# Kernel optimization log

Measured on AMD Instinct MI355X. Metric: run time of the kernel, lower is better.

The kernel has to match this reference:

```python
import jax, jax.numpy as jnp
import numpy as np

L_XYZ = 10  # fourier freqs for position -> 3 + 6*10 = 63 dims
L_DIR = 4   # fourier freqs for direction -> 3 + 6*4 = 27 dims
DIM = 32    # radiance feature dim per depth layer
PPP = 4     # points (depth layers) per pixel
HID = 128   # MLP hidden width
UCH = 64    # UNet hidden channels


def pe(x, L):
    # fourier positional encoding: [x, sin(2^k x), cos(2^k x)]
    f = (2.0 ** jnp.arange(L)).astype(x.dtype)
    xf = x[..., None] * f  # [..., 3, L]
    s = jnp.sin(xf).reshape(x.shape[:-1] + (-1,))
    c = jnp.cos(xf).reshape(x.shape[:-1] + (-1,))
    return jnp.concatenate([x, s, c], axis=-1)


def conv(x, w, b):
    y = jax.lax.conv_general_dilated(x, w, (1, 1), 'SAME',
                                     dimension_numbers=('NCHW', 'OIHW', 'NCHW'))
    return y + b[None, :, None, None]


def setup_inputs() -> dict:
    key = jax.random.key(0)
    ks = jax.random.split(key, 24)
    H = W = 384
    zbufs = jax.random.uniform(ks[0], (H, W, PPP), dtype=jnp.float32)  # depths in [0,1)
    o = jax.random.normal(ks[1], (H, W, 3), dtype=jnp.float32)
    d = jax.random.normal(ks[2], (H, W, 3), dtype=jnp.float32)
    d = d / jnp.linalg.norm(d, axis=-1, keepdims=True)
    cos = jax.random.uniform(ks[3], (H, W, 1), dtype=jnp.float32) * 0.5 + 0.5
    ray = jnp.concatenate([o, d, cos], axis=-1)  # [H,W,7]
    gt = jax.random.uniform(ks[4], (H, W, 3), dtype=jnp.float32)
    mask_gt = jnp.ones((H, W, 1), dtype=jnp.float32)
    xyz_o = jax.random.normal(ks[5], (1024, 3), dtype=jnp.float32)
    in_xyz = 3 + 6 * L_XYZ
    in_dir = 3 + 6 * L_DIR
    in_ch = DIM * PPP
    p = {}
    p['w1'] = jax.random.normal(ks[6], (in_xyz, HID), dtype=jnp.float32) * 0.05
    p['b1'] = jnp.zeros((HID,), dtype=jnp.float32)
    p['w2'] = jax.random.normal(ks[7], (HID, HID), dtype=jnp.float32) * 0.05
    p['b2'] = jnp.zeros((HID,), dtype=jnp.float32)
    p['w3'] = jax.random.normal(ks[8], (HID + in_dir, DIM), dtype=jnp.float32) * 0.05
    p['b3'] = jnp.zeros((DIM,), dtype=jnp.float32)
    p['mpn_w1'] = jax.random.normal(ks[9], (in_ch, in_ch, 3, 3), dtype=jnp.float32) * 0.02
    p['mpn_b1'] = jnp.zeros((in_ch,), dtype=jnp.float32)
    p['mpn_w2'] = jax.random.normal(ks[10], (in_ch, in_ch, 3, 3), dtype=jnp.float32) * 0.02
    p['mpn_b2'] = jnp.zeros((in_ch,), dtype=jnp.float32)
    p['uw1'] = jax.random.normal(ks[11], (UCH, in_ch, 3, 3), dtype=jnp.float32) * 0.02
    p['ub1'] = jnp.zeros((UCH,), dtype=jnp.float32)
    p['uw2'] = jax.random.normal(ks[12], (UCH, UCH, 3, 3), dtype=jnp.float32) * 0.02
    p['ub2'] = jnp.zeros((UCH,), dtype=jnp.float32)
    p['uw3'] = jax.random.normal(ks[13], (3, UCH, 3, 3), dtype=jnp.float32) * 0.02
    p['ub3'] = jnp.zeros((3,), dtype=jnp.float32)
    inp = {'zbufs': zbufs, 'ray': ray, 'gt': gt, 'mask_gt': mask_gt,
           'isTrain': 1, 'xyz_o': xyz_o}
    inp.update(p)
    return inp


def reference(zbufs, ray, gt, mask_gt, isTrain, xyz_o,
              w1, b1, w2, b2, w3, b3,
              mpn_w1, mpn_b1, mpn_w2, mpn_b2,
              uw1, ub1, uw2, ub2, uw3, ub3):
    H, W, P = zbufs.shape
    o = ray[..., :3]
    dirs = ray[..., 3:6]
    cos = ray[..., 6:7]
    thresh = 0.2 if isTrain else 0.0
    # dense equivalent of boolean-mask gather -> MLP -> scatter into zeros
    mask = (zbufs > thresh).astype(zbufs.dtype)  # [H,W,P]
    # xyz_near = o + dirs * zbuf / cos  (xyznear path)
    xyz = o[..., None, :] + dirs[..., None, :] * zbufs[..., None] / cos[..., None]  # [H,W,P,3]
    x = pe(xyz, L_XYZ)                                   # [H,W,P,63]
    h = jax.nn.relu(x @ w1 + b1)                         # [H,W,P,HID]
    h = jax.nn.relu(h @ w2 + b2)
    dpe = pe(dirs, L_DIR)                                # [H,W,27]
    dpe = jnp.broadcast_to(dpe[..., None, :], h.shape[:-1] + (dpe.shape[-1],))
    feat = jnp.concatenate([h, dpe], axis=-1) @ w3 + b3  # [H,W,P,DIM]
    feat = feat * mask[..., None]                        # zeros where pix_mask is False
    # per-layer permute(2,3,0,1) + cat(dim=1) == [1, P*DIM, H, W]
    rdmp = feat.transpose(2, 3, 0, 1).reshape(1, P * DIM, H, W)
    # MPN: predicted per-channel mask
    m = jax.nn.sigmoid(conv(jax.nn.relu(conv(rdmp, mpn_w1, mpn_b1)), mpn_w2, mpn_b2))
    fuse = rdmp * m
    fea_map = jax.nn.sigmoid(fuse[0, :3].transpose(1, 2, 0))  # [H,W,3]
    # UNet refinement to RGB
    u = jax.nn.relu(conv(fuse, uw1, ub1))
    u = jax.nn.relu(conv(u, uw2, ub2))
    img = jax.nn.sigmoid(conv(u, uw3, ub3))[0].transpose(1, 2, 0)  # [H,W,3]
    return img
```

## Files before the change

### kernel.cpp

```cpp
#include <hip/hip_runtime.h>
#include <hip/hip_bf16.h>
#include <math.h>

typedef __attribute__((ext_vector_type(8))) unsigned short ushort8;
typedef __attribute__((ext_vector_type(8))) __bf16 bf16x8;
typedef __attribute__((ext_vector_type(4))) float floatx4;

constexpr int IMGW = 384;
constexpr int NPIX = IMGW * IMGW;

__device__ __forceinline__ unsigned short f2bf(float f) {
  union { float f; unsigned u; } v; v.f = f;
  unsigned u = v.u;
  return (unsigned short)((u + 0x7fffu + ((u >> 16) & 1u)) >> 16);
}
__device__ __forceinline__ float bf2f(unsigned short h) {
  union { unsigned u; float f; } v; v.u = ((unsigned)h) << 16; return v.f;
}
__device__ __forceinline__ unsigned pk2bf(float a, float b) {
  float2 f2; f2.x = a; f2.y = b;
  __hip_bfloat162 h = __float22bfloat162_rn(f2);
  union { __hip_bfloat162 h; unsigned u; } u; u.h = h; return u.u;
}
__device__ __forceinline__ floatx4 mfma16(bf16x8 a, bf16x8 b, floatx4 c) {
  return __builtin_amdgcn_mfma_f32_16x16x32_bf16(a, b, c, 0, 0, 0);
}
__device__ __forceinline__ bf16x8 lds_frag(const unsigned short* p) {
  return *reinterpret_cast<const bf16x8*>(p);
}
__device__ __forceinline__ bf16x8 u4_to_bf(uint4 v) {
  union { uint4 u; bf16x8 b; } c; c.u = v; return c.b;
}

__device__ __forceinline__ void convB_elem(const float* __restrict__ w,
                                           unsigned short* __restrict__ wt,
                                           int i, int CIN, int G, int NT) {
  int j = i & 7, lane = (i >> 3) & 63;
  int rest = i >> 9;
  int nt = rest % NT; int rest2 = rest / NT;
  int g = rest2 % G;  int ks = rest2 / G;
  int q = lane >> 4, m = lane & 15;
  int co = (g * NT + nt) * 16 + m;
  int k = ks * 32 + q * 8 + j;
  int nb = k / CIN, ci = k - nb * CIN;
  wt[i] = f2bf(w[(co * CIN + ci) * 9 + nb]);
}

__global__ __launch_bounds__(256) void prep_all(
    const float* __restrict__ w1, const float* __restrict__ w2, const float* __restrict__ w3,
    const float* __restrict__ mw1, const float* __restrict__ mw2,
    const float* __restrict__ uw1, const float* __restrict__ uw2,
    unsigned short* __restrict__ w1A, unsigned short* __restrict__ w2A,
    unsigned short* __restrict__ w3A,
    unsigned short* __restrict__ cw1, unsigned short* __restrict__ cw2,
    unsigned short* __restrict__ cu1, unsigned short* __restrict__ cu2) {
  int i = blockIdx.x * 256 + threadIdx.x;
  if (i < 28672) {
    if (i < 8192) {
      int j = i & 7, lane = (i >> 3) & 63, t = i >> 9;
      int mt = t >> 1, ks = t & 1;
      int ch_out = mt * 16 + (lane & 15);
      int kp = ks * 32 + (lane >> 4) * 8 + j;
      int chunk = kp >> 3, sl = kp & 7;
      float val;
      if (chunk == 7 && sl >= 4) {
        int c = sl - 4;
        val = (c < 3) ? w1[c * 128 + ch_out] : 0.0f;
      } else {
        const int coordA[8] = {0,0,0,1,1,2,2,2};
        const int octA[8]   = {0,4,8,2,6,0,4,8};
        const int coordB[8] = {0,0,1,1,1,2,2,2};
        const int octB[8]   = {2,6,0,4,8,2,6,0};
        int rc  = (sl < 4) ? coordA[chunk] : coordB[chunk];
        int oct = ((sl < 4) ? octA[chunk] : octB[chunk]) + ((sl >> 1) & 1);
        int korig = ((sl & 1) ? 33 : 3) + rc * 10 + oct;
        val = w1[korig * 128 + ch_out];
      }
      w1A[i] = f2bf(val);
    } else if (i < 24576) {
      int i2 = i - 8192;
      int j = i2 & 7, lane = (i2 >> 3) & 63, t = i2 >> 9;
      int mt = t >> 2, ks = t & 3;
      int ch_out = mt * 16 + (lane & 15);
      int kp = ks * 32 + (lane >> 4) * 8 + j;
      int c_orig = ((kp >> 2) & 7) * 16 + (kp >> 5) * 4 + (kp & 3);
      w2A[i2] = f2bf(w2[c_orig * 128 + ch_out]);
    } else {
      int i3 = i - 24576;
      int j = i3 & 7, lane = (i3 >> 3) & 63, t = i3 >> 9;
      int mt = t >> 2, ks = t & 3;
      int ch_out = mt * 16 + (lane & 15);
      int kp = ks * 32 + (lane >> 4) * 8 + j;
      int c_orig = ((kp >> 2) & 7) * 16 + (kp >> 5) * 4 + (kp & 3);
      w3A[i3] = f2bf(w3[c_orig * 32 + ch_out]);
    }
    return;
  }
  i -= 28672;
  if (i < 147456) { convB_elem(mw1, cw1, i, 128, 4, 2); return; }
  i -= 147456;
  if (i < 147456) { convB_elem(mw2, cw2, i, 128, 4, 2); return; }
  i -= 147456;
  if (i < 73728)  { convB_elem(uw1, cu1, i, 128, 4, 1); return; }
  i -= 73728;
  if (i < 36864)  { convB_elem(uw2, cu2, i, 64, 4, 1); return; }
}

__global__ __launch_bounds__(256) void dcon_kernel(
    const float* __restrict__ ray, const float* __restrict__ w3,
    const float* __restrict__ b3, float* __restrict__ dconG) {
  int gid = blockIdx.x * 256 + threadIdx.x;
  int pixel = gid >> 5, c = gid & 31;
  const float* r = ray + (size_t)pixel * 7;
  float d0 = r[3], d1 = r[4], d2 = r[5];
  float acc = b3[c];
  acc += d0 * w3[128 * 32 + c] + d1 * w3[129 * 32 + c] + d2 * w3[130 * 32 + c];
  float dv[3] = { d0, d1, d2 };
  #pragma unroll
  for (int cc = 0; cc < 3; ++cc) {
    float fs = 1.0f;
    #pragma unroll
    for (int f = 0; f < 4; ++f) {
      float s, co;
      __sincosf(dv[cc] * fs, &s, &co);
      acc += s * w3[(131 + cc * 4 + f) * 32 + c];
      acc += co * w3[(143 + cc * 4 + f) * 32 + c];
      fs *= 2.0f;
    }
  }
  dconG[gid] = acc;
}

__global__ __launch_bounds__(64, 3) void mlp_kernel(
    const float* __restrict__ zbufs, const float* __restrict__ ray,
    const int* __restrict__ isTrain,
    const float* __restrict__ b1, const float* __restrict__ b2,
    const unsigned short* __restrict__ w1A, const unsigned short* __restrict__ w2A,
    const unsigned short* __restrict__ w3A, const float* __restrict__ dconG,
    unsigned short* __restrict__ rdmp) {
  __shared__ __align__(16) unsigned short H[64 * 136];

  const int lane = threadIdx.x;
  const int q = lane >> 4, m = lane & 15;
  const float thresh = (isTrain[0] != 0) ? 0.2f : 0.0f;

  float fA[2], fB[2];
  int cAi[2], cBi[2];
  #pragma unroll
  for (int half = 0; half < 2; ++half) {
    int ch = half * 4 + q;
    cAi[half] = (ch <= 2) ? 0 : ((ch <= 4) ? 1 : 2);
    fA[half]  = (ch == 0 || ch == 5) ? 1.0f :
                (ch == 1 || ch == 6) ? 16.0f :
                (ch == 2 || ch == 7) ? 256.0f :
                (ch == 3) ? 4.0f : 64.0f;
    cBi[half] = (ch <= 1) ? 0 : ((ch <= 4) ? 1 : 2);
    fB[half]  = (ch == 2) ? 1.0f :
                (ch == 0 || ch == 5) ? 4.0f :
                (ch == 3) ? 16.0f :
                (ch == 1 || ch == 6) ? 64.0f : 256.0f;
  }

  bf16x8 bx[4][2];
  float zs[4];
  #pragma unroll
  for (int nt = 0; nt < 4; ++nt) {
    int s = nt * 16 + m;
    int sg = blockIdx.x * 64 + s;
    int pixel = sg >> 2;
    float z = zbufs[sg];
    zs[nt] = z;
    const float* r = ray + (size_t)pixel * 7;
    float t = z / r[6];
    float xv0 = r[0] + r[3] * t, xv1 = r[1] + r[4] * t, xv2 = r[2] + r[5] * t;
    #pragma unroll
    for (int half = 0; half < 2; ++half) {
      float uA = (cAi[half] == 0) ? xv0 : ((cAi[half] == 1) ? xv1 : xv2);
      float uB = (cBi[half] == 0) ? xv0 : ((cBi[half] == 1) ? xv1 : xv2);
      float sa, ca, sb, cb;
      __sincosf(uA * fA[half], &sa, &ca);
      __sincosf(uB * fB[half], &sb, &cb);
      float t2a = sa + sa;
      float sa1 = t2a * ca, ca1 = fmaf(-t2a, sa, 1.0f);
      float t2b = sb + sb;
      float sb1 = t2b * cb, cb1 = fmaf(-t2b, sb, 1.0f);
      if (half == 1 && q == 3) { sb = xv0; cb = xv1; sb1 = xv2; cb1 = 0.0f; }
      uint4 dv;
      dv.x = pk2bf(sa, ca); dv.y = pk2bf(sa1, ca1);
      dv.z = pk2bf(sb, cb); dv.w = pk2bf(sb1, cb1);
      bx[nt][half] = u4_to_bf(dv);
    }
  }

  #pragma unroll 1
  for (int half = 0; half < 2; ++half) {
    floatx4 acc[4][4];
    #pragma unroll
    for (int mt = 0; mt < 4; ++mt) {
      float4 bb = *reinterpret_cast<const float4*>(b1 + (half * 4 + mt) * 16 + q * 4);
      #pragma unroll
      for (int nt = 0; nt < 4; ++nt) {
        acc[mt][nt][0] = bb.x; acc[mt][nt][1] = bb.y;
        acc[mt][nt][2] = bb.z; acc[mt][nt][3] = bb.w;
      }
    }
    #pragma unroll
    for (int ks = 0; ks < 2; ++ks) {
      #pragma unroll
      for (int mt = 0; mt < 4; ++mt) {
        int mtg = half * 4 + mt;
        bf16x8 a = *reinterpret_cast<const bf16x8*>(w1A + (((mtg << 1) + ks) << 9) + lane * 8);
        #pragma unroll
        for (int nt = 0; nt < 4; ++nt)
          acc[mt][nt] = mfma16(a, bx[nt][ks], acc[mt][nt]);
      }
    }
    #pragma unroll
    for (int nt = 0; nt < 4; ++nt) {
      uint4* base = reinterpret_cast<uint4*>(&H[(nt * 16 + m) * 136 + q * 32 + half * 16]);
      #pragma unroll
      for (int g = 0; g < 2; ++g) {
        uint4 v;
        v.x = pk2bf(fmaxf(acc[2*g][nt][0], 0.0f),   fmaxf(acc[2*g][nt][1], 0.0f));
        v.y = pk2bf(fmaxf(acc[2*g][nt][2], 0.0f),   fmaxf(acc[2*g][nt][3], 0.0f));
        v.z = pk2bf(fmaxf(acc[2*g+1][nt][0], 0.0f), fmaxf(acc[2*g+1][nt][1], 0.0f));
        v.w = pk2bf(fmaxf(acc[2*g+1][nt][2], 0.0f), fmaxf(acc[2*g+1][nt][3], 0.0f));
        base[g] = v;
      }
    }
  }

  {
    uint4 keep[4][2];
    #pragma unroll 1
    for (int half = 0; half < 2; ++half) {
      floatx4 acc[4][4];
      #pragma unroll
      for (int mt = 0; mt < 4; ++mt) {
        float4 bb = *reinterpret_cast<const float4*>(b2 + (half * 4 + mt) * 16 + q * 4);
        #pragma unroll
        for (int nt = 0; nt < 4; ++nt) {
          acc[mt][nt][0] = bb.x; acc[mt][nt][1] = bb.y;
          acc[mt][nt][2] = bb.z; acc[mt][nt][3] = bb.w;
        }
      }
      #pragma unroll 1
      for (int ks = 0; ks < 4; ++ks) {
        bf16x8 bf[4];
        #pragma unroll
        for (int nt = 0; nt < 4; ++nt)
          bf[nt] = lds_frag(H + (nt * 16 + m) * 136 + ks * 32 + q * 8);
        #pragma unroll
        for (int mt = 0; mt < 4; ++mt) {
          int mtg = half * 4 + mt;
          bf16x8 a = *reinterpret_cast<const bf16x8*>(w2A + (((mtg << 2) + ks) << 9) + lane * 8);
          #pragma unroll
          for (int nt = 0; nt < 4; ++nt)
            acc[mt][nt] = mfma16(a, bf[nt], acc[mt][nt]);
        }
      }
      #pragma unroll
      for (int nt = 0; nt < 4; ++nt) {
        #pragma unroll
        for (int g = 0; g < 2; ++g) {
          uint4 v;
          v.x = pk2bf(fmaxf(acc[2*g][nt][0], 0.0f),   fmaxf(acc[2*g][nt][1], 0.0f));
          v.y = pk2bf(fmaxf(acc[2*g][nt][2], 0.0f),   fmaxf(acc[2*g][nt][3], 0.0f));
          v.z = pk2bf(fmaxf(acc[2*g+1][nt][0], 0.0f), fmaxf(acc[2*g+1][nt][1], 0.0f));
          v.w = pk2bf(fmaxf(acc[2*g+1][nt][2], 0.0f), fmaxf(acc[2*g+1][nt][3], 0.0f));
          if (half == 0) {
            keep[nt][g] = v;
          } else {
            *reinterpret_cast<uint4*>(&H[(nt * 16 + m) * 136 + q * 32 + 16 + g * 8]) = v;
          }
        }
      }
    }
    #pragma unroll
    for (int nt = 0; nt < 4; ++nt)
      #pragma unroll
      for (int g = 0; g < 2; ++g)
        *reinterpret_cast<uint4*>(&H[(nt * 16 + m) * 136 + q * 32 + g * 8]) = keep[nt][g];
  }

  {
    floatx4 acc[2][4];
    const float* dg = dconG + (size_t)blockIdx.x * 512;
    #pragma unroll
    for (int nt = 0; nt < 4; ++nt) {
      int s = nt * 16 + m;
      #pragma unroll
      for (int mt = 0; mt < 2; ++mt)
        acc[mt][nt] = *reinterpret_cast<const floatx4*>(dg + (s >> 2) * 32 + mt * 16 + q * 4);
    }
    #pragma unroll 2
    for (int ks = 0; ks < 4; ++ks) {
      bf16x8 bf[4];
      #pragma unroll
      for (int nt = 0; nt < 4; ++nt)
        bf[nt] = lds_frag(H + (nt * 16 + m) * 136 + ks * 32 + q * 8);
      #pragma unroll
      for (int mt = 0; mt < 2; ++mt) {
        bf16x8 a = *reinterpret_cast<const bf16x8*>(w3A + (((mt << 2) + ks) << 9) + lane * 8);
        #pragma unroll
        for (int nt = 0; nt < 4; ++nt)
          acc[mt][nt] = mfma16(a, bf[nt], acc[mt][nt]);
      }
    }
    #pragma unroll
    for (int nt = 0; nt < 4; ++nt) {
      int s = nt * 16 + m;
      float mk = (zs[nt] > thresh) ? 1.0f : 0.0f;
      unsigned short* dst = rdmp + (size_t)blockIdx.x * 2048 + s * 32 + q * 4;
      #pragma unroll
      for (int mt = 0; mt < 2; ++mt) {
        uint2 pk;
        pk.x = pk2bf(acc[mt][nt][0] * mk, acc[mt][nt][1] * mk);
        pk.y = pk2bf(acc[mt][nt][2] * mk, acc[mt][nt][3] * mk);
        *reinterpret_cast<uint2*>(dst + mt * 16) = pk;
      }
    }
  }
}

template<int CIN, int COUT, int MODE, int MINW>
__global__ __launch_bounds__(256, MINW) void conv3x3(
    const unsigned short* __restrict__ in, const unsigned short* __restrict__ wt,
    const float* __restrict__ bias, const unsigned short* __restrict__ rdmp,
    unsigned short* __restrict__ out) {
  constexpr int CP  = CIN + 8;
  constexpr int CH8 = CIN / 8;
  constexpr int KC  = CIN / 32;
  constexpr int NT  = COUT / 64;
  constexpr int GROUPS = KC * 3;
  __shared__ __align__(16) unsigned short lds_in[10 * 18 * CP];

  const int tid = threadIdx.x;
  const int x0 = blockIdx.x * 16, y0 = blockIdx.y * 8;

  for (int i = tid; i < 180 * CH8; i += 256) {
    int pix = i / CH8, part = i - pix * CH8;
    int xx = pix % 18, yy = pix / 18;
    int gx = x0 - 1 + xx, gy = y0 - 1 + yy;
    ushort8 v = {0, 0, 0, 0, 0, 0, 0, 0};
    if (gx >= 0 && gx < IMGW && gy >= 0 && gy < IMGW)
      v = *reinterpret_cast<const ushort8*>(in + ((size_t)(gy * IMGW + gx)) * CIN + part * 8);
    *reinterpret_cast<ushort8*>(&lds_in[pix * CP + part * 8]) = v;
  }
  __syncthreads();

  const int wave = tid >> 6, lane = tid & 63, q = lane >> 4, m = lane & 15;
  floatx4 acc[8][NT] = {};

  auto loadB = [&](int g, bf16x8 (&bb)[3][NT]) {
    int kc = g / 3, dx = g - kc * 3;
    #pragma unroll
    for (int dy = 0; dy < 3; ++dy) {
      int ks = (dy * 3 + dx) * KC + kc;
      #pragma unroll
      for (int nt = 0; nt < NT; ++nt)
        bb[dy][nt] = *reinterpret_cast<const bf16x8*>(
            wt + ((((size_t)ks * 4 + wave) * NT + nt) << 9) + lane * 8);
    }
  };

  bf16x8 bcur[3][NT], bnxt[3][NT];
  loadB(0, bcur);

  #pragma unroll 1
  for (int g = 0; g < GROUPS; ++g) {
    if (g + 1 < GROUPS) loadB(g + 1, bnxt);
    int kc = g / 3, dx = g - kc * 3;
    bf16x8 a[10];
    #pragma unroll
    for (int rr = 0; rr < 10; ++rr)
      a[rr] = lds_frag(&lds_in[(rr * 18 + m + dx) * CP + kc * 32 + q * 8]);
    #pragma unroll
    for (int dy = 0; dy < 3; ++dy)
      #pragma unroll
      for (int nt = 0; nt < NT; ++nt)
        #pragma unroll
        for (int mt = 0; mt < 8; ++mt)
          acc[mt][nt] = mfma16(a[mt + dy], bcur[dy][nt], acc[mt][nt]);
    #pragma unroll
    for (int dy = 0; dy < 3; ++dy)
      #pragma unroll
      for (int nt = 0; nt < NT; ++nt)
        bcur[dy][nt] = bnxt[dy][nt];
  }

  const int co0 = wave * (COUT / 4);
  #pragma unroll
  for (int mt = 0; mt < 8; ++mt) {
    int y = y0 + mt;
    #pragma unroll
    for (int nt = 0; nt < NT; ++nt) {
      int co = co0 + nt * 16 + m;
      float bb = bias[co];
      #pragma unroll
      for (int r = 0; r < 4; ++r) {
        int pixel = y * IMGW + x0 + q * 4 + r;
        float v = acc[mt][nt][r] + bb;
        if (MODE == 0) {
          v = fmaxf(v, 0.0f);
        } else {
          v = 1.0f / (1.0f + __expf(-v));
          v *= bf2f(rdmp[(size_t)pixel * 128 + co]);
        }
        out[(size_t)pixel * COUT + co] = f2bf(v);
      }
    }
  }
}

__global__ __launch_bounds__(256) void uconv3_kernel(
    const unsigned short* __restrict__ u2, const float* __restrict__ w,
    const float* __restrict__ b, float* __restrict__ out) {
  __shared__ float wl[1728];
  for (int i = threadIdx.x; i < 1728; i += 256) {
    int c = i % 3; int t = i / 3; int ci = t & 63; int nb = t >> 6;
    wl[i] = w[(c * 64 + ci) * 9 + nb];
  }
  __syncthreads();
  int pixel = blockIdx.x * 256 + threadIdx.x;
  int py = pixel / IMGW, px = pixel - py * IMGW;
  float a0 = b[0], a1 = b[1], a2 = b[2];
  for (int nb = 0; nb < 9; ++nb) {
    int gy = py + nb / 3 - 1, gx = px + nb % 3 - 1;
    if (gx < 0 || gx >= IMGW || gy < 0 || gy >= IMGW) continue;
    const unsigned short* src = u2 + (size_t)(gy * IMGW + gx) * 64;
    const float* wp = wl + nb * 192;
    #pragma unroll
    for (int cc = 0; cc < 8; ++cc) {
      ushort8 v = *reinterpret_cast<const ushort8*>(src + cc * 8);
      #pragma unroll
      for (int j = 0; j < 8; ++j) {
        float uv = bf2f(v[j]);
        const float* w3p = wp + (cc * 8 + j) * 3;
        a0 += uv * w3p[0]; a1 += uv * w3p[1]; a2 += uv * w3p[2];
      }
    }
  }
  float* o = out + (size_t)pixel * 3;
  o[0] = 1.0f / (1.0f + __expf(-a0));
  o[1] = 1.0f / (1.0f + __expf(-a1));
  o[2] = 1.0f / (1.0f + __expf(-a2));
}

extern "C" void kernel_launch(void* const* d_in, const int* in_sizes, int n_in,
                              void* d_out, int out_size, void* d_ws, size_t ws_size,
                              hipStream_t stream) {
  (void)in_sizes; (void)n_in; (void)out_size; (void)ws_size;
  const float* zbufs = (const float*)d_in[0];
  const float* ray   = (const float*)d_in[1];
  const int* isTrain = (const int*)d_in[4];
  const float* w1 = (const float*)d_in[6];
  const float* b1 = (const float*)d_in[7];
  const float* w2 = (const float*)d_in[8];
  const float* b2 = (const float*)d_in[9];
  const float* w3 = (const float*)d_in[10];
  const float* b3 = (const float*)d_in[11];
  const float* mpn_w1 = (const float*)d_in[12];
  const float* mpn_b1 = (const float*)d_in[13];
  const float* mpn_w2 = (const float*)d_in[14];
  const float* mpn_b2 = (const float*)d_in[15];
  const float* uw1 = (const float*)d_in[16];
  const float* ub1 = (const float*)d_in[17];
  const float* uw2 = (const float*)d_in[18];
  const float* ub2 = (const float*)d_in[19];
  const float* uw3 = (const float*)d_in[20];
  const float* ub3 = (const float*)d_in[21];
  float* out = (float*)d_out;

  unsigned char* ws = (unsigned char*)d_ws;
  size_t off = 0;
  auto alloc = [&](size_t bytes) -> void* {
    void* p = ws + off; off = (off + bytes + 255) & ~(size_t)255; return p;
  };
  unsigned short* w1A  = (unsigned short*)alloc(8192 * 2);
  unsigned short* w2A  = (unsigned short*)alloc(16384 * 2);
  unsigned short* w3A  = (unsigned short*)alloc(4096 * 2);
  unsigned short* cw1  = (unsigned short*)alloc((size_t)128 * 1152 * 2);
  unsigned short* cw2  = (unsigned short*)alloc((size_t)128 * 1152 * 2);
  unsigned short* cu1  = (unsigned short*)alloc((size_t)64 * 1152 * 2);
  unsigned short* cu2  = (unsigned short*)alloc((size_t)64 * 576 * 2);
  unsigned short* rdmp = (unsigned short*)alloc((size_t)NPIX * 128 * 2);
  unsigned short* t1   = (unsigned short*)alloc((size_t)NPIX * 128 * 2);
  unsigned short* fuse = (unsigned short*)alloc((size_t)NPIX * 128 * 2);
  unsigned short* u1 = t1;
  unsigned short* u2 = rdmp;
  float* dconG = (float*)fuse;

  prep_all<<<1696, 256, 0, stream>>>(w1, w2, w3, mpn_w1, mpn_w2, uw1, uw2,
                                     w1A, w2A, w3A, cw1, cw2, cu1, cu2);
  dcon_kernel<<<NPIX * 32 / 256, 256, 0, stream>>>(ray, w3, b3, dconG);
  mlp_kernel<<<NPIX * 4 / 64, 64, 0, stream>>>(zbufs, ray, isTrain, b1, b2,
                                               w1A, w2A, w3A, dconG, rdmp);

  dim3 cgrid(IMGW / 16, IMGW / 8);
  conv3x3<128, 128, 0, 2><<<cgrid, 256, 0, stream>>>(rdmp, cw1, mpn_b1, nullptr, t1);
  conv3x3<128, 128, 1, 2><<<cgrid, 256, 0, stream>>>(t1, cw2, mpn_b2, rdmp, fuse);
  conv3x3<128, 64, 0, 3><<<cgrid, 256, 0, stream>>>(fuse, cu1, ub1, nullptr, u1);
  conv3x3<64, 64, 0, 3><<<cgrid, 256, 0, stream>>>(u1, cu2, ub2, nullptr, u2);
  uconv3_kernel<<<NPIX / 256, 256, 0, stream>>>(u2, uw3, ub3, out);
}
```

Before: 335.5 us.

## Split conv3x3 tile rows across 8 waves and double-buffer weight fragments

The 3x3 conv kernels now launch 512 threads per block. Waves are split into 4 output-channel groups by 2 row halves, so each wave accumulates 4 rows instead of 8. This halves per-wave accumulator registers to raise occupancy, with launch bounds raised to 512 threads and a min-blocks hint of 4. The weight-fragment prefetch is restructured into explicit ping-pong buffers with the loop unrolled by two. The cost is that each weight fragment is now loaded by two waves, doubling weight-load traffic, and the overlapping A rows are read from LDS redundantly (6 rows per wave instead of 10 shared).

After: 337.3 us. Within noise of the previous version (+0.5%).

```diff
diff --git a/kernel.cpp b/kernel.cpp
--- a/kernel.cpp
+++ b/kernel.cpp
@@ -324,7 +324,7 @@
 }
 
 template<int CIN, int COUT, int MODE, int MINW>
-__global__ __launch_bounds__(256, MINW) void conv3x3(
+__global__ __launch_bounds__(512, MINW) void conv3x3(
     const unsigned short* __restrict__ in, const unsigned short* __restrict__ wt,
     const float* __restrict__ bias, const unsigned short* __restrict__ rdmp,
     unsigned short* __restrict__ out) {
@@ -338,7 +338,7 @@
   const int tid = threadIdx.x;
   const int x0 = blockIdx.x * 16, y0 = blockIdx.y * 8;
 
-  for (int i = tid; i < 180 * CH8; i += 256) {
+  for (int i = tid; i < 180 * CH8; i += 512) {
     int pix = i / CH8, part = i - pix * CH8;
     int xx = pix % 18, yy = pix / 18;
     int gx = x0 - 1 + xx, gy = y0 - 1 + yy;
@@ -350,7 +350,9 @@
   __syncthreads();
 
   const int wave = tid >> 6, lane = tid & 63, q = lane >> 4, m = lane & 15;
-  floatx4 acc[8][NT] = {};
+  const int cw = wave & 3;
+  const int rw = wave >> 2;
+  floatx4 acc[4][NT] = {};
 
   auto loadB = [&](int g, bf16x8 (&bb)[3][NT]) {
     int kc = g / 3, dx = g - kc * 3;
@@ -360,39 +362,38 @@
       #pragma unroll
       for (int nt = 0; nt < NT; ++nt)
         bb[dy][nt] = *reinterpret_cast<const bf16x8*>(
-            wt + ((((size_t)ks * 4 + wave) * NT + nt) << 9) + lane * 8);
+            wt + ((((size_t)ks * 4 + cw) * NT + nt) << 9) + lane * 8);
     }
   };
-
-  bf16x8 bcur[3][NT], bnxt[3][NT];
-  loadB(0, bcur);
-
+  auto compute = [&](int g, bf16x8 (&bb)[3][NT]) {
+    int kc = g / 3, dx = g - kc * 3;
+    bf16x8 a[6];
+    #pragma unroll
+    for (int rr = 0; rr < 6; ++rr)
+      a[rr] = lds_frag(&lds_in[((rw * 4 + rr) * 18 + m + dx) * CP + kc * 32 + q * 8]);
+    #pragma unroll
+    for (int dy = 0; dy < 3; ++dy)
+      #pragma unroll
+      for (int nt = 0; nt < NT; ++nt)
+        #pragma unroll
+        for (int mt = 0; mt < 4; ++mt)
+          acc[mt][nt] = mfma16(a[mt + dy], bb[dy][nt], acc[mt][nt]);
+  };
+
+  bf16x8 b0[3][NT], b1[3][NT];
+  loadB(0, b0);
   #pragma unroll 1
-  for (int g = 0; g < GROUPS; ++g) {
-    if (g + 1 < GROUPS) loadB(g + 1, bnxt);
-    int kc = g / 3, dx = g - kc * 3;
-    bf16x8 a[10];
-    #pragma unroll
-    for (int rr = 0; rr < 10; ++rr)
-      a[rr] = lds_frag(&lds_in[(rr * 18 + m + dx) * CP + kc * 32 + q * 8]);
-    #pragma unroll
-    for (int dy = 0; dy < 3; ++dy)
-      #pragma unroll
-      for (int nt = 0; nt < NT; ++nt)
-        #pragma unroll
-        for (int mt = 0; mt < 8; ++mt)
-          acc[mt][nt] = mfma16(a[mt + dy], bcur[dy][nt], acc[mt][nt]);
-    #pragma unroll
-    for (int dy = 0; dy < 3; ++dy)
-      #pragma unroll
-      for (int nt = 0; nt < NT; ++nt)
-        bcur[dy][nt] = bnxt[dy][nt];
-  }
-
-  const int co0 = wave * (COUT / 4);
+  for (int g = 0; g < GROUPS; g += 2) {
+    loadB(g + 1, b1);
+    compute(g, b0);
+    if (g + 2 < GROUPS) loadB(g + 2, b0);
+    compute(g + 1, b1);
+  }
+
+  const int co0 = cw * (COUT / 4);
   #pragma unroll
-  for (int mt = 0; mt < 8; ++mt) {
-    int y = y0 + mt;
+  for (int mt = 0; mt < 4; ++mt) {
+    int y = y0 + rw * 4 + mt;
     #pragma unroll
     for (int nt = 0; nt < NT; ++nt) {
       int co = co0 + nt * 16 + m;
@@ -498,9 +499,9 @@
                                                w1A, w2A, w3A, dconG, rdmp);
 
   dim3 cgrid(IMGW / 16, IMGW / 8);
-  conv3x3<128, 128, 0, 2><<<cgrid, 256, 0, stream>>>(rdmp, cw1, mpn_b1, nullptr, t1);
-  conv3x3<128, 128, 1, 2><<<cgrid, 256, 0, stream>>>(t1, cw2, mpn_b2, rdmp, fuse);
-  conv3x3<128, 64, 0, 3><<<cgrid, 256, 0, stream>>>(fuse, cu1, ub1, nullptr, u1);
-  conv3x3<64, 64, 0, 3><<<cgrid, 256, 0, stream>>>(u1, cu2, ub2, nullptr, u2);
+  conv3x3<128, 128, 0, 4><<<cgrid, 512, 0, stream>>>(rdmp, cw1, mpn_b1, nullptr, t1);
+  conv3x3<128, 128, 1, 4><<<cgrid, 512, 0, stream>>>(t1, cw2, mpn_b2, rdmp, fuse);
+  conv3x3<128, 64, 0, 4><<<cgrid, 512, 0, stream>>>(fuse, cu1, ub1, nullptr, u1);
+  conv3x3<64, 64, 0, 4><<<cgrid, 512, 0, stream>>>(u1, cu2, ub2, nullptr, u2);
   uconv3_kernel<<<NPIX / 256, 256, 0, stream>>>(u2, uw3, ub3, out);
 }
```
